# Performance work log

Measured on AMD Instinct MI355X. Metric: run time of the kernel, lower is better.

## Reference

```python
import jax, jax.numpy as jnp
import numpy as np

K = 128        # numClass
PUW = 1.0      # puW from __init__
EPS = 0.01     # the +0.01 clamp inside log(1 - p + 0.01)


def setup_inputs() -> dict:
    key = jax.random.key(0)
    k1, k2, k3 = jax.random.split(key, 3)
    N = 262144
    outputs = jax.random.normal(k1, (N, K), dtype=jnp.float32)
    # labels in [0, K]; label == K means 'unlabeled' (goes to U set)
    labels = jax.random.randint(k2, (N,), 0, K + 1, dtype=jnp.int64)
    priorlist = jax.random.uniform(k3, (K,), dtype=jnp.float32)
    indexlist = jnp.arange(32, dtype=jnp.int64)  # the 32 labeled classes
    return {"outputs": outputs, "labels": labels,
            "priorlist": priorlist, "indexlist": indexlist}


def reference(outputs, labels, priorlist, indexlist):
    outputs = outputs.astype(jnp.float32)
    s = jax.nn.softmax(outputs, axis=1)                      # [N, K]

    maskP = (labels <= K - 1)                                # positive (labeled)
    maskU = jnp.logical_not(maskP)                           # unlabeled
    fP = maskP.astype(jnp.float32)
    fU = maskU.astype(jnp.float32)
    nP = jnp.maximum(jnp.float32(1.0), fP.sum())
    nU = jnp.maximum(jnp.float32(1.0), fU.sum())

    neglog = -jnp.log(1.0 - s + EPS)                         # [N, K]
    sumU = jnp.sum(neglog * fU[:, None], axis=0)             # [K] sums over U rows
    sumP = jnp.sum(neglog * fP[:, None], axis=0)             # [K] sums over P rows

    L = indexlist.shape[0]
    in_idx = jnp.zeros((K,), dtype=bool).at[indexlist].set(True)

    # classes in indexlist: pu3; classes not in indexlist: pu1
    pu3 = jnp.sum(jnp.where(in_idx, sumU, 0.0)) / nU / L
    pu1 = (jnp.sum(jnp.where(in_idx, 0.0, sumP))
           * priorlist[indexlist[0]] / nP / (K - L))

    # pu2: per positive sample, -log(1 - p[label] + eps) * prior[label]
    lab_c = jnp.clip(labels, 0, K - 1)
    gathered = jnp.take_along_axis(neglog, lab_c[:, None], axis=1)[:, 0]
    pu2 = jnp.sum(gathered * priorlist[lab_c] * fP) / nP

    PULoss = pu3 + pu1 - pu2

    # mean cross-entropy over positive samples only
    logp = jax.nn.log_softmax(outputs, axis=1)
    ce_per = -jnp.take_along_axis(logp, lab_c[:, None], axis=1)[:, 0]
    crossloss = jnp.sum(ce_per * fP) / nP

    objective = crossloss
    return (objective, PULoss * PUW, crossloss)
```

## Files before the change

### kernel.cpp

```cpp
#include <hip/hip_runtime.h>
#include <math.h>

#define KCLS 128
#define NBLK 1024


__global__ __launch_bounds__(256) void pu_main(
    const float* __restrict__ outp, const int* __restrict__ labels,
    const int* __restrict__ idxlist, const float* __restrict__ prior,
    float* __restrict__ part, int N, int L)
{
    __shared__ __align__(16) float s_notin[KCLS];
    __shared__ __align__(16) float s_prior[KCLS];
    const int tid = threadIdx.x;
    if (tid < KCLS) { s_prior[tid] = prior[tid]; s_notin[tid] = 1.0f; }
    __syncthreads();
    if (tid < L) s_notin[idxlist[tid]] = 0.0f;
    __syncthreads();

    const int lane  = tid & 63;
    const int wave  = tid >> 6;
    const int half  = lane >> 5;
    const int hlane = lane & 31;
    const int globalWave = blockIdx.x * (blockDim.x >> 6) + wave;
    const int numWaves   = NBLK * (256 >> 6);

    const float4 nm4 = ((const float4*)s_notin)[hlane];
    const float4 in4 = make_float4(1.f - nm4.x, 1.f - nm4.y,
                                   1.f - nm4.z, 1.f - nm4.w);
    const float4 pr4 = ((const float4*)s_prior)[hlane];

    float aU = 0.f, aP = 0.f, aPu2 = 0.f, aCE = 0.f, cP = 0.f, cU = 0.f;

    auto process = [&](float4 o4, int lab) {
        const bool isP  = (lab < KCLS);
        const int  labc = isP ? lab : (KCLS - 1);

        const float e0 = __expf(o4.x), e1 = __expf(o4.y),
                    e2 = __expf(o4.z), e3 = __expf(o4.w);
        float psum = (e0 + e1) + (e2 + e3);
        #pragma unroll
        for (int off = 16; off; off >>= 1)
            psum += __shfl_xor(psum, off);
        const float inv = __builtin_amdgcn_rcpf(psum);

        const float s0 = e0 * inv, s1 = e1 * inv, s2 = e2 * inv, s3 = e3 * inv;
        const float nl0 = -__logf((1.0f - s0) + 0.01f);
        const float nl1 = -__logf((1.0f - s1) + 0.01f);
        const float nl2 = -__logf((1.0f - s2) + 0.01f);
        const float nl3 = -__logf((1.0f - s3) + 0.01f);

        const float vP = isP ? 1.f : 0.f;
        const float vU = 1.f - vP;

        aP += vP * ((nl0 * nm4.x + nl1 * nm4.y) + (nl2 * nm4.z + nl3 * nm4.w));
        aU += vU * ((nl0 * in4.x + nl1 * in4.y) + (nl2 * in4.z + nl3 * in4.w));

        if ((labc >> 2) == hlane) {
            const int sub = labc & 3;
            const float olab = (sub == 0) ? o4.x : (sub == 1) ? o4.y : (sub == 2) ? o4.z : o4.w;
            const float nll  = (sub == 0) ? nl0  : (sub == 1) ? nl1  : (sub == 2) ? nl2  : nl3;
            const float prl  = (sub == 0) ? pr4.x : (sub == 1) ? pr4.y : (sub == 2) ? pr4.z : pr4.w;
            aPu2 += vP * nll * prl;
            aCE  += vP * (__logf(psum) - olab);
        }
        if (hlane == 0) { cP += vP; cU += vU; }
    };

    const int npairs = N >> 1;
    int pair = globalWave;
    for (; pair + numWaves < npairs; pair += 2 * numWaves) {
        const int rowA = pair * 2 + half;
        const int rowB = (pair + numWaves) * 2 + half;
        const float4 oA = ((const float4*)(outp + (size_t)rowA * KCLS))[hlane];
        const int    lA = labels[rowA];
        const float4 oB = ((const float4*)(outp + (size_t)rowB * KCLS))[hlane];
        const int    lB = labels[rowB];
        process(oA, lA);
        process(oB, lB);
    }
    for (; pair < npairs; pair += numWaves) {
        const int row = pair * 2 + half;
        const float4 o = ((const float4*)(outp + (size_t)row * KCLS))[hlane];
        process(o, labels[row]);
    }

    #pragma unroll
    for (int off = 32; off; off >>= 1) {
        aU   += __shfl_xor(aU, off);
        aP   += __shfl_xor(aP, off);
        aPu2 += __shfl_xor(aPu2, off);
        aCE  += __shfl_xor(aCE, off);
        cP   += __shfl_xor(cP, off);
        cU   += __shfl_xor(cU, off);
    }

    __shared__ float s_red[4][6];
    if (lane == 0) {
        s_red[wave][0] = aU;  s_red[wave][1] = aP;   s_red[wave][2] = aPu2;
        s_red[wave][3] = aCE; s_red[wave][4] = cP;   s_red[wave][5] = cU;
    }
    __syncthreads();
    if (tid < 6) {
        float t = s_red[0][tid] + s_red[1][tid] + s_red[2][tid] + s_red[3][tid];
        part[tid * NBLK + blockIdx.x] = t;
    }
}

__global__ __launch_bounds__(256) void pu_final(
    const float* __restrict__ part, const float* __restrict__ prior,
    const int* __restrict__ idxlist, float* __restrict__ out, int L)
{
    const int tid  = threadIdx.x;
    const int lane = tid & 63;
    const int wave = tid >> 6;

    double loc[6] = {0, 0, 0, 0, 0, 0};
    for (int b = tid; b < NBLK; b += 256) {
        #pragma unroll
        for (int c = 0; c < 6; ++c) loc[c] += (double)part[c * NBLK + b];
    }
    #pragma unroll
    for (int off = 32; off; off >>= 1) {
        #pragma unroll
        for (int c = 0; c < 6; ++c) loc[c] += __shfl_xor(loc[c], off);
    }
    __shared__ double s_red[4][6];
    if (lane == 0) {
        #pragma unroll
        for (int c = 0; c < 6; ++c) s_red[wave][c] = loc[c];
    }
    __syncthreads();
    if (tid == 0) {
        const double aU   = s_red[0][0] + s_red[1][0] + s_red[2][0] + s_red[3][0];
        const double aP   = s_red[0][1] + s_red[1][1] + s_red[2][1] + s_red[3][1];
        const double aPu2 = s_red[0][2] + s_red[1][2] + s_red[2][2] + s_red[3][2];
        const double aCE  = s_red[0][3] + s_red[1][3] + s_red[2][3] + s_red[3][3];
        const double cP   = s_red[0][4] + s_red[1][4] + s_red[2][4] + s_red[3][4];
        const double cU   = s_red[0][5] + s_red[1][5] + s_red[2][5] + s_red[3][5];
        const double nP = cP > 1.0 ? cP : 1.0;
        const double nU = cU > 1.0 ? cU : 1.0;

        const double pu3 = aU / nU / (double)L;
        const double pu1 = aP * (double)prior[idxlist[0]] / nP / (double)(KCLS - L);
        const double pu2 = aPu2 / nP;
        const double ce  = aCE / nP;

        out[0] = (float)ce;
        out[1] = (float)(pu3 + pu1 - pu2);
        out[2] = (float)ce;
    }
}

extern "C" void kernel_launch(void* const* d_in, const int* in_sizes, int n_in,
                              void* d_out, int out_size, void* d_ws, size_t ws_size,
                              hipStream_t stream)
{
    const float* outp   = (const float*)d_in[0];
    const int*   labels = (const int*)d_in[1];
    const float* prior  = (const float*)d_in[2];
    const int*   idxl   = (const int*)d_in[3];
    const int N = in_sizes[1];
    const int L = in_sizes[3];

    float* part = (float*)d_ws;

    pu_main<<<NBLK, 256, 0, stream>>>(outp, labels, idxl, prior, part, N, L);
    pu_final<<<1, 256, 0, stream>>>(part, prior, idxl, (float*)d_out, L);
}
```

Before: 196.2 us.

## Process rows with 16 lanes and replace per-element logs with log of products

Result: no change. 197.3 us (+0.5%).

```diff
diff --git a/kernel.cpp b/kernel.cpp
--- a/kernel.cpp
+++ b/kernel.cpp
@@ -20,69 +20,90 @@
 
     const int lane  = tid & 63;
     const int wave  = tid >> 6;
-    const int half  = lane >> 5;
-    const int hlane = lane & 31;
-    const int globalWave = blockIdx.x * (blockDim.x >> 6) + wave;
-    const int numWaves   = NBLK * (256 >> 6);
+    const int seg   = lane >> 4;
+    const int slane = lane & 15;
+    const int base  = slane * 8;
+    const int globalWave = blockIdx.x * 4 + wave;
+    const int numWaves   = NBLK * 4;
 
-    const float4 nm4 = ((const float4*)s_notin)[hlane];
-    const float4 in4 = make_float4(1.f - nm4.x, 1.f - nm4.y,
-                                   1.f - nm4.z, 1.f - nm4.w);
-    const float4 pr4 = ((const float4*)s_prior)[hlane];
+    const float4 nmA = ((const float4*)s_notin)[2 * slane];
+    const float4 nmB = ((const float4*)s_notin)[2 * slane + 1];
+    const float4 inA = make_float4(1.f - nmA.x, 1.f - nmA.y, 1.f - nmA.z, 1.f - nmA.w);
+    const float4 inB = make_float4(1.f - nmB.x, 1.f - nmB.y, 1.f - nmB.z, 1.f - nmB.w);
+    const float4 prA = ((const float4*)s_prior)[2 * slane];
+    const float4 prB = ((const float4*)s_prior)[2 * slane + 1];
 
     float aU = 0.f, aP = 0.f, aPu2 = 0.f, aCE = 0.f, cP = 0.f, cU = 0.f;
 
-    auto process = [&](float4 o4, int lab) {
+    auto process = [&](float4 oA, float4 oB, int lab) {
         const bool isP  = (lab < KCLS);
         const int  labc = isP ? lab : (KCLS - 1);
 
-        const float e0 = __expf(o4.x), e1 = __expf(o4.y),
-                    e2 = __expf(o4.z), e3 = __expf(o4.w);
-        float psum = (e0 + e1) + (e2 + e3);
+        const float e0 = __expf(oA.x), e1 = __expf(oA.y), e2 = __expf(oA.z), e3 = __expf(oA.w);
+        const float e4 = __expf(oB.x), e5 = __expf(oB.y), e6 = __expf(oB.z), e7 = __expf(oB.w);
+        float psum = ((e0 + e1) + (e2 + e3)) + ((e4 + e5) + (e6 + e7));
         #pragma unroll
-        for (int off = 16; off; off >>= 1)
+        for (int off = 8; off; off >>= 1)
             psum += __shfl_xor(psum, off);
         const float inv = __builtin_amdgcn_rcpf(psum);
 
-        const float s0 = e0 * inv, s1 = e1 * inv, s2 = e2 * inv, s3 = e3 * inv;
-        const float nl0 = -__logf((1.0f - s0) + 0.01f);
-        const float nl1 = -__logf((1.0f - s1) + 0.01f);
-        const float nl2 = -__logf((1.0f - s2) + 0.01f);
-        const float nl3 = -__logf((1.0f - s3) + 0.01f);
+        const float d0 = fmaf(-e0, inv, 0.01f), d1 = fmaf(-e1, inv, 0.01f);
+        const float d2 = fmaf(-e2, inv, 0.01f), d3 = fmaf(-e3, inv, 0.01f);
+        const float d4 = fmaf(-e4, inv, 0.01f), d5 = fmaf(-e5, inv, 0.01f);
+        const float d6 = fmaf(-e6, inv, 0.01f), d7 = fmaf(-e7, inv, 0.01f);
+
+        const float pN =
+            ((fmaf(nmA.x, d0, 1.f) * fmaf(nmA.y, d1, 1.f)) *
+             (fmaf(nmA.z, d2, 1.f) * fmaf(nmA.w, d3, 1.f))) *
+            ((fmaf(nmB.x, d4, 1.f) * fmaf(nmB.y, d5, 1.f)) *
+             (fmaf(nmB.z, d6, 1.f) * fmaf(nmB.w, d7, 1.f)));
+        const float pI =
+            ((fmaf(inA.x, d0, 1.f) * fmaf(inA.y, d1, 1.f)) *
+             (fmaf(inA.z, d2, 1.f) * fmaf(inA.w, d3, 1.f))) *
+            ((fmaf(inB.x, d4, 1.f) * fmaf(inB.y, d5, 1.f)) *
+             (fmaf(inB.z, d6, 1.f) * fmaf(inB.w, d7, 1.f)));
 
         const float vP = isP ? 1.f : 0.f;
         const float vU = 1.f - vP;
+        aP -= vP * __logf(pN);
+        aU -= vU * __logf(pI);
 
-        aP += vP * ((nl0 * nm4.x + nl1 * nm4.y) + (nl2 * nm4.z + nl3 * nm4.w));
-        aU += vU * ((nl0 * in4.x + nl1 * in4.y) + (nl2 * in4.z + nl3 * in4.w));
+        const int rel = labc - base;
+        const float m0 = (rel == 0) ? 1.f : 0.f, m1 = (rel == 1) ? 1.f : 0.f;
+        const float m2 = (rel == 2) ? 1.f : 0.f, m3 = (rel == 3) ? 1.f : 0.f;
+        const float m4 = (rel == 4) ? 1.f : 0.f, m5 = (rel == 5) ? 1.f : 0.f;
+        const float m6 = (rel == 6) ? 1.f : 0.f, m7 = (rel == 7) ? 1.f : 0.f;
+        const float fown = ((unsigned)rel < 8u) ? 1.f : 0.f;
 
-        if ((labc >> 2) == hlane) {
-            const int sub = labc & 3;
-            const float olab = (sub == 0) ? o4.x : (sub == 1) ? o4.y : (sub == 2) ? o4.z : o4.w;
-            const float nll  = (sub == 0) ? nl0  : (sub == 1) ? nl1  : (sub == 2) ? nl2  : nl3;
-            const float prl  = (sub == 0) ? pr4.x : (sub == 1) ? pr4.y : (sub == 2) ? pr4.z : pr4.w;
-            aPu2 += vP * nll * prl;
-            aCE  += vP * (__logf(psum) - olab);
-        }
-        if (hlane == 0) { cP += vP; cU += vU; }
+        const float dsel = (m0*d0 + m1*d1 + m2*d2 + m3*d3) + (m4*d4 + m5*d5 + m6*d6 + m7*d7);
+        const float osel = (m0*oA.x + m1*oA.y + m2*oA.z + m3*oA.w)
+                         + (m4*oB.x + m5*oB.y + m6*oB.z + m7*oB.w);
+        const float prsl = (m0*prA.x + m1*prA.y + m2*prA.z + m3*prA.w)
+                         + (m4*prB.x + m5*prB.y + m6*prB.z + m7*prB.w);
+
+        aPu2 -= vP * prsl * __logf(1.0f + dsel);
+        aCE  += vP * (fown * __logf(psum) - osel);
+        if (slane == 0) { cP += vP; cU += vU; }
     };
 
-    const int npairs = N >> 1;
-    int pair = globalWave;
-    for (; pair + numWaves < npairs; pair += 2 * numWaves) {
-        const int rowA = pair * 2 + half;
-        const int rowB = (pair + numWaves) * 2 + half;
-        const float4 oA = ((const float4*)(outp + (size_t)rowA * KCLS))[hlane];
+    const int nquads = N >> 2;
+    int q = globalWave;
+    for (; q + numWaves < nquads; q += 2 * numWaves) {
+        const int rowA = q * 4 + seg;
+        const int rowB = (q + numWaves) * 4 + seg;
+        const float4* rpA = (const float4*)(outp + (size_t)rowA * KCLS);
+        const float4* rpB = (const float4*)(outp + (size_t)rowB * KCLS);
+        const float4 a1 = rpA[2 * slane], a2 = rpA[2 * slane + 1];
         const int    lA = labels[rowA];
-        const float4 oB = ((const float4*)(outp + (size_t)rowB * KCLS))[hlane];
+        const float4 b1 = rpB[2 * slane], b2 = rpB[2 * slane + 1];
         const int    lB = labels[rowB];
-        process(oA, lA);
-        process(oB, lB);
+        process(a1, a2, lA);
+        process(b1, b2, lB);
     }
-    for (; pair < npairs; pair += numWaves) {
-        const int row = pair * 2 + half;
-        const float4 o = ((const float4*)(outp + (size_t)row * KCLS))[hlane];
-        process(o, labels[row]);
+    for (; q < nquads; q += numWaves) {
+        const int row = q * 4 + seg;
+        const float4* rp = (const float4*)(outp + (size_t)row * KCLS);
+        process(rp[2 * slane], rp[2 * slane + 1], labels[row]);
     }
 
     #pragma unroll
```
